# Kernel tuning notes

Measured on AMD Instinct MI355X. Metric: run time of the kernel, lower is better.

## Reference

```python
import jax, jax.numpy as jnp
import numpy as np

N_VEH = 40000
N_PATH = 400000
N_ACTOR = 128
N_MAP = 128
ACT_C = 32
PAT_C = 32
SIZE = N_ACTOR + N_MAP + ACT_C + PAT_C  # 320
HID = SIZE // 2  # 160
EPS = 1e-5


def _gn1(x, w, b):
    # GroupNorm with 1 group over channel dim of [N, C]: per-row normalize, per-channel affine
    mu = jnp.mean(x, axis=-1, keepdims=True)
    var = jnp.mean(jnp.square(x - mu), axis=-1, keepdims=True)
    return (x - mu) * jax.lax.rsqrt(var + EPS) * w + b


def setup_inputs() -> dict:
    key = jax.random.key(0)
    ks = jax.random.split(key, 12)
    inp = {
        "actors": jax.random.normal(ks[0], (N_VEH, N_ACTOR), jnp.float32),
        "paths": jax.random.normal(ks[1], (N_PATH, N_MAP), jnp.float32),
        "Z_act": jax.random.normal(ks[2], (N_VEH, ACT_C), jnp.float32),
        "Z_pat": jax.random.normal(ks[3], (N_PATH, PAT_C), jnp.float32),
        "u": jax.random.randint(ks[4], (N_PATH,), 0, N_VEH, jnp.int64 if jax.config.jax_enable_x64 else jnp.int32),
        # LinRes params (LaneGCN LinearRes: Linear(bias=False) -> GN -> ReLU -> Linear(bias=False) -> GN -> +transform(x) -> ReLU)
        "w1": jax.random.normal(ks[5], (HID, SIZE), jnp.float32) / np.sqrt(SIZE),
        "w2": jax.random.normal(ks[6], (HID, HID), jnp.float32) / np.sqrt(HID),
        "wt": jax.random.normal(ks[7], (HID, SIZE), jnp.float32) / np.sqrt(SIZE),
        "g1w": jnp.ones((HID,), jnp.float32),
        "g1b": jnp.zeros((HID,), jnp.float32),
        "g2w": jnp.ones((HID,), jnp.float32),
        "g2b": jnp.zeros((HID,), jnp.float32),
        # final head Linear(HID, 1)
        "wh": jax.random.normal(ks[8], (1, HID), jnp.float32) / np.sqrt(HID),
        "bh": jnp.zeros((1,), jnp.float32),
    }
    return inp


def reference(actors, paths, Z_act, Z_pat, u, w1, w2, wt, g1w, g1b, g2w, g2b, wh, bh):
    # edge-indexed gather + concat: [N_PATH, SIZE]
    x = jnp.concatenate([paths, Z_pat, actors[u], Z_act[u]], axis=-1)
    h = jnp.einsum('ns,hs->nh', x, w1)
    h = jax.nn.relu(_gn1(h, g1w, g1b))
    h = jnp.einsum('nh,gh->ng', h, w2)
    h = _gn1(h, g2w, g2b)
    h = jax.nn.relu(h + jnp.einsum('ns,hs->nh', x, wt))
    logits = jnp.einsum('nh,oh->no', h, wh) + bh
    return logits
```

## Files before the change

### kernel.cpp

```cpp
#include <hip/hip_runtime.h>
#include <hip/hip_bf16.h>

typedef short short8 __attribute__((ext_vector_type(8)));
typedef float floatx4 __attribute__((ext_vector_type(4)));

#define XP 328
#define HP 168

__device__ __forceinline__ unsigned short f2bf(float f) {
    __hip_bfloat16 h = __float2bfloat16(f);
    return __builtin_bit_cast(unsigned short, h);
}
__device__ __forceinline__ float bf2f(unsigned short s) {
    __hip_bfloat16 h = __builtin_bit_cast(__hip_bfloat16, s);
    return __bfloat162float(h);
}

__global__ void pack_wc(const float* __restrict__ w1, const float* __restrict__ wt,
                        unsigned short* __restrict__ dst) {
    int i = blockIdx.x * 256 + threadIdx.x;
    if (i >= 320 * 320) return;
    int j = i & 7;
    int lane = (i >> 3) & 63;
    int r = i >> 9;
    int kb = r % 10;
    int t = r / 10;
    int n = t * 16 + (lane & 15);
    int k = kb * 32 + ((lane >> 4) << 3) + j;
    float v = (n < 160) ? w1[n * 320 + k] : wt[(n - 160) * 320 + k];
    dst[i] = f2bf(v);
}

__global__ void pack_w2(const float* __restrict__ w2, unsigned short* __restrict__ dst) {
    int i = blockIdx.x * 256 + threadIdx.x;
    if (i >= 160 * 160) return;
    int j = i & 7;
    int lane = (i >> 3) & 63;
    int r = i >> 9;
    int kb = r % 5;
    int t = r / 5;
    int n = t * 16 + (lane & 15);
    int k = kb * 32 + ((lane >> 4) << 3) + j;
    dst[i] = f2bf(w2[n * 160 + k]);
}

__global__ __launch_bounds__(128, 3) void fused_kernel(
    const float* __restrict__ actors, const float* __restrict__ paths,
    const float* __restrict__ Z_act, const float* __restrict__ Z_pat,
    const int* __restrict__ u,
    const unsigned short* __restrict__ pB1, const unsigned short* __restrict__ pB2,
    const float* __restrict__ g1w, const float* __restrict__ g1b,
    const float* __restrict__ g2w, const float* __restrict__ g2b,
    const float* __restrict__ wh, const float* __restrict__ bh,
    float* __restrict__ out)
{
    __shared__ __align__(16) char smem[21504];
    unsigned short* lX  = (unsigned short*)smem;
    unsigned short* lH1 = (unsigned short*)smem;
    unsigned short* lHT = (unsigned short*)(smem + 10752);

    const int tid  = threadIdx.x;
    const int wave = tid >> 6;
    const int lane = tid & 63;
    const int quad = lane >> 4;
    const int l15  = lane & 15;
    const int row0 = blockIdx.x * 32;

    float4 vD[10], vG[10];
    int uv[10];
    #pragma unroll
    for (int i = 0; i < 10; i++) {
        int f = i * 128 + tid;
        int r = f / 40, q = f - r * 40;
        const float* src = (q < 32) ? (paths + (size_t)(row0 + r) * 128 + q * 4)
                                    : (Z_pat + (size_t)(row0 + r) * 32 + (q - 32) * 4);
        vD[i] = *(const float4*)src;
        uv[i] = u[row0 + r];
    }
    #pragma unroll
    for (int i = 0; i < 10; i++) {
        int f = i * 128 + tid;
        int q = f % 40;
        int un = uv[i];
        const float* src = (q < 32) ? (actors + (size_t)un * 128 + q * 4)
                                    : (Z_act + (size_t)un * 32 + (q - 32) * 4);
        vG[i] = *(const float4*)src;
    }
    #pragma unroll
    for (int i = 0; i < 10; i++) {
        int f = i * 128 + tid;
        int r = f / 40, q = f - r * 40;
        ushort4 sv;
        sv.x = f2bf(vD[i].x); sv.y = f2bf(vD[i].y); sv.z = f2bf(vD[i].z); sv.w = f2bf(vD[i].w);
        *(ushort4*)(lX + r * XP + q * 4) = sv;
    }
    #pragma unroll
    for (int i = 0; i < 10; i++) {
        int f = i * 128 + tid;
        int r = f / 40, q = f - r * 40;
        ushort4 sv;
        sv.x = f2bf(vG[i].x); sv.y = f2bf(vG[i].y); sv.z = f2bf(vG[i].z); sv.w = f2bf(vG[i].w);
        *(ushort4*)(lX + r * XP + 160 + q * 4) = sv;
    }

    short8 bC[10], bN[10];
    #pragma unroll
    for (int ti = 0; ti < 10; ti++) {
        int t = wave * 10 + ti;
        bC[ti] = *(const short8*)(pB1 + ((size_t)(t * 10 + 0) * 64 + lane) * 8);
    }
    __syncthreads();

    floatx4 fzero = {0.f, 0.f, 0.f, 0.f};
    floatx4 acc[2][10];
    #pragma unroll
    for (int i = 0; i < 2; i++)
        #pragma unroll
        for (int j = 0; j < 10; j++) acc[i][j] = fzero;

    #pragma unroll
    for (int kb = 0; kb < 10; kb++) {
        short8 a[2];
        #pragma unroll
        for (int mt = 0; mt < 2; mt++)
            a[mt] = *(const short8*)(lX + (mt * 16 + l15) * XP + kb * 32 + quad * 8);
        if (kb < 9) {
            #pragma unroll
            for (int ti = 0; ti < 10; ti++) {
                int t = wave * 10 + ti;
                bN[ti] = *(const short8*)(pB1 + ((size_t)(t * 10 + kb + 1) * 64 + lane) * 8);
            }
        }
        #pragma unroll
        for (int ti = 0; ti < 10; ti++)
            #pragma unroll
            for (int mt = 0; mt < 2; mt++)
                acc[mt][ti] = __builtin_amdgcn_mfma_f32_16x16x32_bf16(a[mt], bC[ti], acc[mt][ti], 0, 0, 0);
        #pragma unroll
        for (int ti = 0; ti < 10; ti++) bC[ti] = bN[ti];
    }
    __syncthreads();

    if (wave == 0) {
        float s[8], q2[8];
        #pragma unroll
        for (int mt = 0; mt < 2; mt++)
            #pragma unroll
            for (int r = 0; r < 4; r++) {
                float sv = 0.f, qv = 0.f;
                #pragma unroll
                for (int ti = 0; ti < 10; ti++) {
                    float v = acc[mt][ti][r];
                    sv += v; qv += v * v;
                }
                s[mt * 4 + r] = sv; q2[mt * 4 + r] = qv;
            }
        #pragma unroll
        for (int off = 1; off <= 8; off <<= 1)
            #pragma unroll
            for (int k = 0; k < 8; k++) {
                s[k]  += __shfl_xor(s[k],  off, 64);
                q2[k] += __shfl_xor(q2[k], off, 64);
            }
        float gw[10], gb[10];
        #pragma unroll
        for (int ti = 0; ti < 10; ti++) {
            int n = ti * 16 + l15;
            gw[ti] = g1w[n]; gb[ti] = g1b[n];
        }
        #pragma unroll
        for (int mt = 0; mt < 2; mt++)
            #pragma unroll
            for (int r = 0; r < 4; r++) {
                float mu = s[mt * 4 + r] * (1.f / 160.f);
                float var = q2[mt * 4 + r] * (1.f / 160.f) - mu * mu;
                float rs = rsqrtf(var + 1e-5f);
                int m = mt * 16 + quad * 4 + r;
                #pragma unroll
                for (int ti = 0; ti < 10; ti++) {
                    float v = (acc[mt][ti][r] - mu) * rs * gw[ti] + gb[ti];
                    v = fmaxf(v, 0.f);
                    lH1[m * HP + ti * 16 + l15] = f2bf(v);
                }
            }
    } else {
        #pragma unroll
        for (int mt = 0; mt < 2; mt++)
            #pragma unroll
            for (int ti = 0; ti < 10; ti++)
                #pragma unroll
                for (int r = 0; r < 4; r++) {
                    int m = mt * 16 + quad * 4 + r;
                    lHT[m * HP + ti * 16 + l15] = f2bf(acc[mt][ti][r]);
                }
    }

    short8 b2C[10], b2N[10];
    #pragma unroll
    for (int ti = 0; ti < 10; ti++)
        b2C[ti] = *(const short8*)(pB2 + ((size_t)(ti * 5 + 0) * 64 + lane) * 8);
    __syncthreads();

    floatx4 acc2[10];
    #pragma unroll
    for (int j = 0; j < 10; j++) acc2[j] = fzero;

    #pragma unroll
    for (int kb = 0; kb < 5; kb++) {
        short8 a = *(const short8*)(lH1 + (wave * 16 + l15) * HP + kb * 32 + quad * 8);
        if (kb < 4) {
            #pragma unroll
            for (int ti = 0; ti < 10; ti++)
                b2N[ti] = *(const short8*)(pB2 + ((size_t)(ti * 5 + kb + 1) * 64 + lane) * 8);
        }
        #pragma unroll
        for (int ti = 0; ti < 10; ti++)
            acc2[ti] = __builtin_amdgcn_mfma_f32_16x16x32_bf16(a, b2C[ti], acc2[ti], 0, 0, 0);
        #pragma unroll
        for (int ti = 0; ti < 10; ti++) b2C[ti] = b2N[ti];
    }

    {
        float s[4], q2[4];
        #pragma unroll
        for (int r = 0; r < 4; r++) {
            float sv = 0.f, qv = 0.f;
            #pragma unroll
            for (int ti = 0; ti < 10; ti++) {
                float v = acc2[ti][r];
                sv += v; qv += v * v;
            }
            s[r] = sv; q2[r] = qv;
        }
        #pragma unroll
        for (int off = 1; off <= 8; off <<= 1)
            #pragma unroll
            for (int r = 0; r < 4; r++) {
                s[r]  += __shfl_xor(s[r],  off, 64);
                q2[r] += __shfl_xor(q2[r], off, 64);
            }
        float g2wv[10], g2bv[10], whv[10];
        #pragma unroll
        for (int ti = 0; ti < 10; ti++) {
            int n = ti * 16 + l15;
            g2wv[ti] = g2w[n]; g2bv[ti] = g2b[n]; whv[ti] = wh[n];
        }
        float dp[4];
        #pragma unroll
        for (int r = 0; r < 4; r++) {
            float mu = s[r] * (1.f / 160.f);
            float var = q2[r] * (1.f / 160.f) - mu * mu;
            float rs = rsqrtf(var + 1e-5f);
            int m = wave * 16 + quad * 4 + r;
            float d = 0.f;
            #pragma unroll
            for (int ti = 0; ti < 10; ti++) {
                float v = (acc2[ti][r] - mu) * rs * g2wv[ti] + g2bv[ti];
                v += bf2f(lHT[m * HP + ti * 16 + l15]);
                v = fmaxf(v, 0.f);
                d += v * whv[ti];
            }
            dp[r] = d;
        }
        #pragma unroll
        for (int off = 1; off <= 8; off <<= 1)
            #pragma unroll
            for (int r = 0; r < 4; r++) dp[r] += __shfl_xor(dp[r], off, 64);
        if (l15 == 0) {
            float bh0 = bh[0];
            #pragma unroll
            for (int r = 0; r < 4; r++)
                out[row0 + wave * 16 + quad * 4 + r] = dp[r] + bh0;
        }
    }
}

extern "C" void kernel_launch(void* const* d_in, const int* in_sizes, int n_in,
                              void* d_out, int out_size, void* d_ws, size_t ws_size,
                              hipStream_t stream) {
    const float* actors = (const float*)d_in[0];
    const float* paths  = (const float*)d_in[1];
    const float* Z_act  = (const float*)d_in[2];
    const float* Z_pat  = (const float*)d_in[3];
    const int*   u      = (const int*)d_in[4];
    const float* w1     = (const float*)d_in[5];
    const float* w2     = (const float*)d_in[6];
    const float* wt     = (const float*)d_in[7];
    const float* g1w    = (const float*)d_in[8];
    const float* g1b    = (const float*)d_in[9];
    const float* g2w    = (const float*)d_in[10];
    const float* g2b    = (const float*)d_in[11];
    const float* wh     = (const float*)d_in[12];
    const float* bh     = (const float*)d_in[13];
    float* out = (float*)d_out;

    unsigned short* pB1 = (unsigned short*)d_ws;
    unsigned short* pB2 = pB1 + 320 * 320;

    hipLaunchKernelGGL(pack_wc, dim3(400), dim3(256), 0, stream, w1, wt, pB1);
    hipLaunchKernelGGL(pack_w2, dim3(100), dim3(256), 0, stream, w2, pB2);
    hipLaunchKernelGGL(fused_kernel, dim3(400000 / 32), dim3(128), 0, stream,
                       actors, paths, Z_act, Z_pat, u, pB1, pB2,
                       g1w, g1b, g2w, g2b, wh, bh, out);
}
```

Measured before the change: 568.2 us.

## Split 32-row tile across four waves with 2x2 M/N partition and swizzled LDS

```diff
diff --git a/kernel.cpp b/kernel.cpp
--- a/kernel.cpp
+++ b/kernel.cpp
@@ -4,7 +4,6 @@
 typedef short short8 __attribute__((ext_vector_type(8)));
 typedef float floatx4 __attribute__((ext_vector_type(4)));
 
-#define XP 328
 #define HP 168
 
 __device__ __forceinline__ unsigned short f2bf(float f) {
@@ -44,7 +43,7 @@
     dst[i] = f2bf(w2[n * 160 + k]);
 }
 
-__global__ __launch_bounds__(128, 3) void fused_kernel(
+__global__ __launch_bounds__(256, 4) void fused_kernel(
     const float* __restrict__ actors, const float* __restrict__ paths,
     const float* __restrict__ Z_act, const float* __restrict__ Z_pat,
     const int* __restrict__ u,
@@ -54,10 +53,13 @@
     const float* __restrict__ wh, const float* __restrict__ bh,
     float* __restrict__ out)
 {
-    __shared__ __align__(16) char smem[21504];
+    __shared__ __align__(16) char smem[21760];
     unsigned short* lX  = (unsigned short*)smem;
     unsigned short* lH1 = (unsigned short*)smem;
     unsigned short* lHT = (unsigned short*)(smem + 10752);
+    float* sS = (float*)(smem + 20992);
+    float* sQ = sS + 64;
+    float* sD = sS + 128;
 
     const int tid  = threadIdx.x;
     const int wave = tid >> 6;
@@ -65,12 +67,14 @@
     const int quad = lane >> 4;
     const int l15  = lane & 15;
     const int row0 = blockIdx.x * 32;
-
-    float4 vD[10], vG[10];
-    int uv[10];
-    #pragma unroll
-    for (int i = 0; i < 10; i++) {
-        int f = i * 128 + tid;
+    const int ms = wave & 1;
+    const int ns = wave >> 1;
+
+    float4 vD[5], vG[5];
+    int uv[5];
+    #pragma unroll
+    for (int i = 0; i < 5; i++) {
+        int f = i * 256 + tid;
         int r = f / 40, q = f - r * 40;
         const float* src = (q < 32) ? (paths + (size_t)(row0 + r) * 128 + q * 4)
                                     : (Z_pat + (size_t)(row0 + r) * 32 + (q - 32) * 4);
@@ -78,8 +82,8 @@
         uv[i] = u[row0 + r];
     }
     #pragma unroll
-    for (int i = 0; i < 10; i++) {
-        int f = i * 128 + tid;
+    for (int i = 0; i < 5; i++) {
+        int f = i * 256 + tid;
         int q = f % 40;
         int un = uv[i];
         const float* src = (q < 32) ? (actors + (size_t)un * 128 + q * 4)
@@ -87,80 +91,70 @@
         vG[i] = *(const float4*)src;
     }
     #pragma unroll
-    for (int i = 0; i < 10; i++) {
-        int f = i * 128 + tid;
+    for (int i = 0; i < 5; i++) {
+        int f = i * 256 + tid;
         int r = f / 40, q = f - r * 40;
+        int g = q >> 1, sub = q & 1;
+        int addr = r * 320 + (((g ^ (r & 7)) << 3) + (sub << 2));
         ushort4 sv;
         sv.x = f2bf(vD[i].x); sv.y = f2bf(vD[i].y); sv.z = f2bf(vD[i].z); sv.w = f2bf(vD[i].w);
-        *(ushort4*)(lX + r * XP + q * 4) = sv;
-    }
-    #pragma unroll
-    for (int i = 0; i < 10; i++) {
-        int f = i * 128 + tid;
+        *(ushort4*)(lX + addr) = sv;
+    }
+    #pragma unroll
+    for (int i = 0; i < 5; i++) {
+        int f = i * 256 + tid;
         int r = f / 40, q = f - r * 40;
+        int g = 20 + (q >> 1), sub = q & 1;
+        int addr = r * 320 + (((g ^ (r & 7)) << 3) + (sub << 2));
         ushort4 sv;
         sv.x = f2bf(vG[i].x); sv.y = f2bf(vG[i].y); sv.z = f2bf(vG[i].z); sv.w = f2bf(vG[i].w);
-        *(ushort4*)(lX + r * XP + 160 + q * 4) = sv;
-    }
-
-    short8 bC[10], bN[10];
-    #pragma unroll
-    for (int ti = 0; ti < 10; ti++) {
-        int t = wave * 10 + ti;
-        bC[ti] = *(const short8*)(pB1 + ((size_t)(t * 10 + 0) * 64 + lane) * 8);
+        *(ushort4*)(lX + addr) = sv;
     }
     __syncthreads();
 
     floatx4 fzero = {0.f, 0.f, 0.f, 0.f};
-    floatx4 acc[2][10];
-    #pragma unroll
-    for (int i = 0; i < 2; i++)
-        #pragma unroll
-        for (int j = 0; j < 10; j++) acc[i][j] = fzero;
-
+    floatx4 acc[10];
+    #pragma unroll
+    for (int j = 0; j < 10; j++) acc[j] = fzero;
+
+    const int arow = ms * 16 + l15;
     #pragma unroll
     for (int kb = 0; kb < 10; kb++) {
-        short8 a[2];
-        #pragma unroll
-        for (int mt = 0; mt < 2; mt++)
-            a[mt] = *(const short8*)(lX + (mt * 16 + l15) * XP + kb * 32 + quad * 8);
-        if (kb < 9) {
+        short8 a = *(const short8*)(lX + arow * 320 + (((kb * 4 + quad) ^ (arow & 7)) << 3));
+        short8 b[5];
+        #pragma unroll
+        for (int ti = 0; ti < 5; ti++)
+            b[ti] = *(const short8*)(pB1 + ((size_t)((ns * 10 + ti) * 10 + kb) * 64 + lane) * 8);
+        #pragma unroll
+        for (int ti = 0; ti < 5; ti++)
+            acc[ti] = __builtin_amdgcn_mfma_f32_16x16x32_bf16(a, b[ti], acc[ti], 0, 0, 0);
+        #pragma unroll
+        for (int ti = 0; ti < 5; ti++)
+            b[ti] = *(const short8*)(pB1 + ((size_t)((ns * 10 + 5 + ti) * 10 + kb) * 64 + lane) * 8);
+        #pragma unroll
+        for (int ti = 0; ti < 5; ti++)
+            acc[5 + ti] = __builtin_amdgcn_mfma_f32_16x16x32_bf16(a, b[ti], acc[5 + ti], 0, 0, 0);
+    }
+    __syncthreads();
+
+    if (ns == 0) {
+        float s[4], q2[4];
+        #pragma unroll
+        for (int r = 0; r < 4; r++) {
+            float sv = 0.f, qv = 0.f;
             #pragma unroll
             for (int ti = 0; ti < 10; ti++) {
-                int t = wave * 10 + ti;
-                bN[ti] = *(const short8*)(pB1 + ((size_t)(t * 10 + kb + 1) * 64 + lane) * 8);
-            }
-        }
-        #pragma unroll
-        for (int ti = 0; ti < 10; ti++)
-            #pragma unroll
-            for (int mt = 0; mt < 2; mt++)
-                acc[mt][ti] = __builtin_amdgcn_mfma_f32_16x16x32_bf16(a[mt], bC[ti], acc[mt][ti], 0, 0, 0);
-        #pragma unroll
-        for (int ti = 0; ti < 10; ti++) bC[ti] = bN[ti];
-    }
-    __syncthreads();
-
-    if (wave == 0) {
-        float s[8], q2[8];
-        #pragma unroll
-        for (int mt = 0; mt < 2; mt++)
+                float v = acc[ti][r];
+                sv += v; qv += v * v;
+            }
+            s[r] = sv; q2[r] = qv;
+        }
+        #pragma unroll
+        for (int off = 1; off <= 8; off <<= 1)
             #pragma unroll
             for (int r = 0; r < 4; r++) {
-                float sv = 0.f, qv = 0.f;
-                #pragma unroll
-                for (int ti = 0; ti < 10; ti++) {
-                    float v = acc[mt][ti][r];
-                    sv += v; qv += v * v;
-                }
-                s[mt * 4 + r] = sv; q2[mt * 4 + r] = qv;
-            }
-        #pragma unroll
-        for (int off = 1; off <= 8; off <<= 1)
-            #pragma unroll
-            for (int k = 0; k < 8; k++) {
-                s[k]  += __shfl_xor(s[k],  off, 64);
-                q2[k] += __shfl_xor(q2[k], off, 64);
+                s[r]  += __shfl_xor(s[r],  off, 64);
+                q2[r] += __shfl_xor(q2[r], off, 64);
             }
         float gw[10], gb[10];
         #pragma unroll
@@ -169,55 +163,40 @@
             gw[ti] = g1w[n]; gb[ti] = g1b[n];
         }
         #pragma unroll
-        for (int mt = 0; mt < 2; mt++)
-            #pragma unroll
-            for (int r = 0; r < 4; r++) {
-                float mu = s[mt * 4 + r] * (1.f / 160.f);
-                float var = q2[mt * 4 + r] * (1.f / 160.f) - mu * mu;
-                float rs = rsqrtf(var + 1e-5f);
-                int m = mt * 16 + quad * 4 + r;
-                #pragma unroll
-                for (int ti = 0; ti < 10; ti++) {
-                    float v = (acc[mt][ti][r] - mu) * rs * gw[ti] + gb[ti];
-                    v = fmaxf(v, 0.f);
-                    lH1[m * HP + ti * 16 + l15] = f2bf(v);
-                }
-            }
+        for (int r = 0; r < 4; r++) {
+            float mu = s[r] * (1.f / 160.f);
+            float var = q2[r] * (1.f / 160.f) - mu * mu;
+            float rs = rsqrtf(var + 1e-5f);
+            int m = ms * 16 + quad * 4 + r;
+            #pragma unroll
+            for (int ti = 0; ti < 10; ti++) {
+                float v = (acc[ti][r] - mu) * rs * gw[ti] + gb[ti];
+                v = fmaxf(v, 0.f);
+                lH1[m * HP + ti * 16 + l15] = f2bf(v);
+            }
+        }
     } else {
         #pragma unroll
-        for (int mt = 0; mt < 2; mt++)
-            #pragma unroll
-            for (int ti = 0; ti < 10; ti++)
-                #pragma unroll
-                for (int r = 0; r < 4; r++) {
-                    int m = mt * 16 + quad * 4 + r;
-                    lHT[m * HP + ti * 16 + l15] = f2bf(acc[mt][ti][r]);
-                }
-    }
-
-    short8 b2C[10], b2N[10];
-    #pragma unroll
-    for (int ti = 0; ti < 10; ti++)
-        b2C[ti] = *(const short8*)(pB2 + ((size_t)(ti * 5 + 0) * 64 + lane) * 8);
-    __syncthreads();
-
-    floatx4 acc2[10];
-    #pragma unroll
-    for (int j = 0; j < 10; j++) acc2[j] = fzero;
-
+        for (int ti = 0; ti < 10; ti++)
+            #pragma unroll
+            for (int r = 0; r < 4; r++)
+                lHT[(((ms * 10 + ti) * 4 + r) << 6) + lane] = f2bf(acc[ti][r]);
+    }
+    __syncthreads();
+
+    floatx4 acc2[5];
+    #pragma unroll
+    for (int j = 0; j < 5; j++) acc2[j] = fzero;
     #pragma unroll
     for (int kb = 0; kb < 5; kb++) {
-        short8 a = *(const short8*)(lH1 + (wave * 16 + l15) * HP + kb * 32 + quad * 8);
-        if (kb < 4) {
-            #pragma unroll
-            for (int ti = 0; ti < 10; ti++)
-                b2N[ti] = *(const short8*)(pB2 + ((size_t)(ti * 5 + kb + 1) * 64 + lane) * 8);
-        }
-        #pragma unroll
-        for (int ti = 0; ti < 10; ti++)
-            acc2[ti] = __builtin_amdgcn_mfma_f32_16x16x32_bf16(a, b2C[ti], acc2[ti], 0, 0, 0);
-        #pragma unroll
-        for (int ti = 0; ti < 10; ti++) b2C[ti] = b2N[ti];
+        short8 a = *(const short8*)(lH1 + (ms * 16 + l15) * HP + kb * 32 + quad * 8);
+        short8 b[5];
+        #pragma unroll
+        for (int ti = 0; ti < 5; ti++)
+            b[ti] = *(const short8*)(pB2 + ((size_t)((ns * 5 + ti) * 5 + kb) * 64 + lane) * 8);
+        #pragma unroll
+        for (int ti = 0; ti < 5; ti++)
+            acc2[ti] = __builtin_amdgcn_mfma_f32_16x16x32_bf16(a, b[ti], acc2[ti], 0, 0, 0);
     }
 
     {
@@ -226,7 +205,7 @@
         for (int r = 0; r < 4; r++) {
             float sv = 0.f, qv = 0.f;
             #pragma unroll
-            for (int ti = 0; ti < 10; ti++) {
+            for (int ti = 0; ti < 5; ti++) {
                 float v = acc2[ti][r];
                 sv += v; qv += v * v;
             }
@@ -239,24 +218,38 @@
                 s[r]  += __shfl_xor(s[r],  off, 64);
                 q2[r] += __shfl_xor(q2[r], off, 64);
             }
-        float g2wv[10], g2bv[10], whv[10];
-        #pragma unroll
-        for (int ti = 0; ti < 10; ti++) {
-            int n = ti * 16 + l15;
+        if (l15 == 0) {
+            #pragma unroll
+            for (int r = 0; r < 4; r++) {
+                int m = ms * 16 + quad * 4 + r;
+                sS[ns * 32 + m] = s[r];
+                sQ[ns * 32 + m] = q2[r];
+            }
+        }
+    }
+    __syncthreads();
+
+    {
+        float g2wv[5], g2bv[5], whv[5];
+        #pragma unroll
+        for (int ti = 0; ti < 5; ti++) {
+            int n = ns * 80 + ti * 16 + l15;
             g2wv[ti] = g2w[n]; g2bv[ti] = g2b[n]; whv[ti] = wh[n];
         }
         float dp[4];
         #pragma unroll
         for (int r = 0; r < 4; r++) {
-            float mu = s[r] * (1.f / 160.f);
-            float var = q2[r] * (1.f / 160.f) - mu * mu;
+            int m = ms * 16 + quad * 4 + r;
+            float ts = sS[m] + sS[32 + m];
+            float tq = sQ[m] + sQ[32 + m];
+            float mu = ts * (1.f / 160.f);
+            float var = tq * (1.f / 160.f) - mu * mu;
             float rs = rsqrtf(var + 1e-5f);
-            int m = wave * 16 + quad * 4 + r;
             float d = 0.f;
             #pragma unroll
-            for (int ti = 0; ti < 10; ti++) {
+            for (int ti = 0; ti < 5; ti++) {
                 float v = (acc2[ti][r] - mu) * rs * g2wv[ti] + g2bv[ti];
-                v += bf2f(lHT[m * HP + ti * 16 + l15]);
+                v += bf2f(lHT[(((ms * 10 + ns * 5 + ti) * 4 + r) << 6) + lane]);
                 v = fmaxf(v, 0.f);
                 d += v * whv[ti];
             }
@@ -267,12 +260,13 @@
             #pragma unroll
             for (int r = 0; r < 4; r++) dp[r] += __shfl_xor(dp[r], off, 64);
         if (l15 == 0) {
-            float bh0 = bh[0];
             #pragma unroll
             for (int r = 0; r < 4; r++)
-                out[row0 + wave * 16 + quad * 4 + r] = dp[r] + bh0;
-        }
-    }
+                sD[ns * 32 + ms * 16 + quad * 4 + r] = dp[r];
+        }
+    }
+    __syncthreads();
+    if (tid < 32) out[row0 + tid] = sD[tid] + sD[32 + tid] + bh[0];
 }
 
 extern "C" void kernel_launch(void* const* d_in, const int* in_sizes, int n_in,
@@ -299,7 +293,7 @@
 
     hipLaunchKernelGGL(pack_wc, dim3(400), dim3(256), 0, stream, w1, wt, pB1);
     hipLaunchKernelGGL(pack_w2, dim3(100), dim3(256), 0, stream, w2, pB2);
-    hipLaunchKernelGGL(fused_kernel, dim3(400000 / 32), dim3(128), 0, stream,
+    hipLaunchKernelGGL(fused_kernel, dim3(400000 / 32), dim3(256), 0, stream,
                        actors, paths, Z_act, Z_pat, u, pB1, pB2,
                        g1w, g1b, g2w, g2b, wh, bh, out);
 }
```

After: 570.3 us. Within noise of the previous version (+0.4%).
